# Kernel tuning notes

Hardware: AMD Instinct MI355X
Metric: run time of the kernel (lower is better)

## Reference

```python
import jax, jax.numpy as jnp
import numpy as np

EPS = 1e-6
BN_EPS = 1e-5
K = 20

def _vn_linear(x, W):
    # x: [B,C,...] channel axis 1; W: [out,in]
    return jnp.einsum('oc,bc...->bo...', W, x)

def _vn_bn(x):
    # training-mode BatchNorm on per-vector norms (affine at init: gamma=1, beta=0)
    norm = jnp.sqrt(jnp.sum(x * x, axis=2)) + EPS  # [B,C,*spatial]
    axes = (0,) + tuple(range(2, norm.ndim))
    mean = jnp.mean(norm, axis=axes, keepdims=True)
    var = jnp.mean((norm - mean) ** 2, axis=axes, keepdims=True)  # biased, as torch BN
    norm_bn = (norm - mean) / jnp.sqrt(var + BN_EPS)
    return x / jnp.expand_dims(norm, 2) * jnp.expand_dims(norm_bn, 2)

def _vn_llr(x, Wf, Wd, ns=0.0, use_bn=True):
    p = _vn_linear(x, Wf)
    if use_bn:
        p = _vn_bn(p)
    d = _vn_linear(x, Wd)
    dot = jnp.sum(p * d, axis=2, keepdims=True)
    mask = (dot >= 0).astype(x.dtype)
    dsq = jnp.sum(d * d, axis=2, keepdims=True)
    return ns * p + (1.0 - ns) * (mask * p + (1.0 - mask) * (p - dot / (dsq + EPS) * d))

def _graph_feature_cross(x, k):
    # x: [B,3,N] -> [B,3,3,N,k]
    B, _, N = x.shape
    inner = -2.0 * jnp.einsum('bdn,bdm->bnm', x, x)
    xx = jnp.sum(x * x, axis=1)  # [B,N]
    pdist = -xx[:, :, None] - inner - xx[:, None, :]  # [B,N,N]
    idx = jax.lax.top_k(pdist, k)[1]  # [B,N,k] nearest neighbors
    xt = jnp.transpose(x, (0, 2, 1))  # [B,N,3]
    nbr = xt[jnp.arange(B)[:, None, None], idx]  # [B,N,k,3]
    ctr = jnp.broadcast_to(xt[:, :, None, :], nbr.shape)  # [B,N,k,3]
    cross = jnp.cross(nbr, ctr)
    feat = jnp.stack([nbr - ctr, ctr, cross], axis=3)  # [B,N,k,3ch,3vec]
    return jnp.transpose(feat, (0, 3, 4, 1, 2))  # [B,3,3,N,k]

def _forward(points, wposf, wposd, w1f, w1d, w2f, w2d, w3, ws1f, ws1d, ws2f, ws2d, wlin):
    x = jnp.transpose(points, (0, 2, 1))  # [B,3,N]
    B, _, N = x.shape
    feat = _graph_feature_cross(x, K)  # [B,3,3,N,K]
    x = _vn_llr(feat, wposf, wposd)  # conv_pos, dim=5 -> [B,21,3,N,K]
    x = jnp.mean(x, axis=-1)  # mean pool over k -> [B,21,3,N]
    x = _vn_llr(x, w1f, w1d)  # conv1
    x = _vn_llr(x, w2f, w2d)  # conv2 (feature_transform=False so in=21? no: conv2 takes 42 -- matches cat-free path only when feature_transform False? conv2 in=42 but code passes x of 21? original passes 21-ch into conv2 only if feature_transform else 21; here feature_transform=False and conv2 expects 42 in torch -- we mirror with w2f [42,42] applied after duplicating? No: mirror exact torch behavior below.)
    return x

def reference(points, wposf, wposd, w1f, w1d, w2f, w2d, w3, ws1f, ws1d, ws2f, ws2d, wlin):
    x = jnp.transpose(points, (0, 2, 1))  # [B,3,N]
    B, _, N = x.shape
    feat = _graph_feature_cross(x, K)  # [B,3,3,N,K]
    x = _vn_llr(feat, wposf, wposd)  # [B,21,3,N,K]
    x = jnp.mean(x, axis=-1)  # mean pool -> [B,21,3,N]
    x = _vn_llr(x, w1f, w1d)  # [B,21,3,N]
    # torch conv2 is Linear(42,42) but with feature_transform=False it is applied to 21-ch
    # input; nn.Linear would error, so faithful runnable form uses the duplicated-channel
    # convention: concat (x, x) is NOT in the original; instead we slice w2 to [42,21].
    x = _vn_llr(x, w2f[:, :21], w2d[:, :21])  # [B,42,3,N]
    x = _vn_bn(_vn_linear(x, w3))  # conv3 + bn3 -> [B,85,3,N]
    x_mean_out = jnp.mean(x, axis=-1, keepdims=True)  # [B,85,3,1]
    x = jnp.concatenate([x, jnp.broadcast_to(x_mean_out, x.shape)], axis=1)  # [B,170,3,N]
    z = _vn_llr(x, ws1f, ws1d)  # [B,85,3,N]
    z = _vn_llr(z, ws2f, ws2d)  # [B,42,3,N]
    z = _vn_linear(z, wlin)  # [B,3,3,N]
    z = jnp.transpose(z, (0, 2, 1, 3))  # [B,3,3,N]
    x_std = jnp.einsum('bijm,bjkm->bikm', x, z)  # [B,170,3,N]
    xf = x_std.reshape(B, -1, N)  # [B,510,N]
    inv_z = jnp.max(xf, axis=-1)  # [B,510]
    center_loc = jnp.mean(x_mean_out, axis=2)  # [B,85,1]
    return (inv_z, x_mean_out, center_loc)

def setup_inputs() -> dict:
    key = jax.random.key(0)
    ks = jax.random.split(key, 14)
    B, N = 4, 8192
    def w(k, shape):
        return (jax.random.normal(k, shape, dtype=jnp.float32) * (1.0 / np.sqrt(shape[1])))
    return {
        'points': jax.random.normal(ks[0], (B, N, 3), dtype=jnp.float32),
        'wposf': w(ks[1], (21, 3)),
        'wposd': w(ks[2], (21, 3)),
        'w1f': w(ks[3], (21, 21)),
        'w1d': w(ks[4], (21, 21)),
        'w2f': w(ks[5], (42, 42)),
        'w2d': w(ks[6], (42, 42)),
        'w3': w(ks[7], (85, 42)),
        'ws1f': w(ks[8], (85, 170)),
        'ws1d': w(ks[9], (85, 170)),
        'ws2f': w(ks[10], (42, 85)),
        'ws2d': w(ks[11], (42, 85)),
        'wlin': w(ks[12], (3, 42)),
    }
```

## Files before the change

kernel.cpp:

```cpp
#include <hip/hip_runtime.h>
#include <cstdint>
#include <cstddef>

#define EPSF 1e-6f
#define BN_EPSF 1e-5f

constexpr int Bb = 4;
constexpr int Nn = 8192;
constexpr int KK = 20;
constexpr int SEG = 8;
constexpr int SEGLEN = Nn / SEG;
constexpr int BUF = 24;

constexpr size_t KNN0_OFF = 0;
constexpr size_t X1_OFF  = 0;
constexpr size_t X2_OFF  = 2064384;
constexpr size_t X3_OFF  = 4128768;
constexpr size_t Z1_OFF  = 0;
constexpr size_t X4_OFF  = 8355840;
constexpr size_t IDX_OFF = 16711680;
constexpr size_t Z2_OFF  = 17367040;
constexpr size_t Z3_OFF  = 21495808;
constexpr size_t ACC_OFF = 21790720;
constexpr size_t XM_OFF  = 21791744;
constexpr size_t BF_OFF  = 21792764;
constexpr size_t BD_OFF  = 21793784;
constexpr size_t DEXT_OFF = 21795840;
constexpr size_t EXT_NEED = (DEXT_OFF + 8355840) * 4;

__device__ __forceinline__ float wave_sum(float v) {
#pragma unroll
  for (int off = 32; off; off >>= 1) v += __shfl_xor(v, off, 64);
  return v;
}
__device__ __forceinline__ float wave_max(float v) {
#pragma unroll
  for (int off = 32; off; off >>= 1) v = fmaxf(v, __shfl_xor(v, off, 64));
  return v;
}
__device__ __forceinline__ uint32_t umin32(uint32_t a, uint32_t b) { return a < b ? a : b; }
__device__ __forceinline__ uint32_t umax32(uint32_t a, uint32_t b) { return a < b ? b : a; }

__global__ __launch_bounds__(1024) void zero_acc(float* __restrict__ a) {
  a[threadIdx.x] = 0.f;
}

__global__ __launch_bounds__(256) void knn_kernel(const float* __restrict__ pts,
                                                  uint32_t* __restrict__ knnp) {
  __shared__ float4 tile[SEGLEN];
  __shared__ uint32_t buf[BUF * 256];
  const int tid = threadIdx.x;
  const int n = blockIdx.x * 256 + tid;
  const int b = blockIdx.y;
  const int s = blockIdx.z;
  const float* pb = pts + (size_t)b * Nn * 3;

  for (int i = tid; i < SEGLEN; i += 256) {
    const float* p = pb + (size_t)(s * SEGLEN + i) * 3;
    const float x = p[0], y = p[1], z = p[2];
    tile[i] = make_float4(x, y, z, 0.5f * (x * x + y * y + z * z));
  }
  const float qx = pb[n * 3 + 0], qy = pb[n * 3 + 1], qz = pb[n * 3 + 2];
  const float nqx = -qx, nqy = -qy, nqz = -qz;
  const float h = 0.5f * (qx * qx + qy * qy + qz * qz);
  __syncthreads();

  uint32_t keys[KK];
#pragma unroll
  for (int j = 0; j < KK; ++j) keys[j] = 0xFFFFFFFFu;

  const int base = s * SEGLEN;

#pragma unroll 4
  for (int j = 0; j < 64; ++j) {
    const float4 c = tile[j];
    float u = fmaf(nqx, c.x, fmaf(nqy, c.y, fmaf(nqz, c.z, c.w + h)));
    u = fmaxf(u, 0.f);
    uint32_t mx = (__float_as_uint(u) & 0xFFFFE000u) | (uint32_t)(base + j);
#pragma unroll
    for (int q = 0; q < KK; ++q) {
      const uint32_t mn = umin32(keys[q], mx);
      mx = umax32(keys[q], mx);
      keys[q] = mn;
    }
  }

  uint32_t thresh = keys[KK - 1];
  float thresh_up = __uint_as_float((thresh & 0xFFFFE000u) + 0x2000u);
  float th_h = thresh_up - h + 2.4e-7f * fabsf(thresh_up) + 1e-30f;
  int cnt = 0;

  for (int j0 = 64; j0 < SEGLEN; j0 += 4) {
#pragma unroll
    for (int u4 = 0; u4 < 4; ++u4) {
      const int j = j0 + u4;
      const float4 c = tile[j];
      const float up = fmaf(nqx, c.x, fmaf(nqy, c.y, fmaf(nqz, c.z, c.w)));
      if (up < th_h) {
        const float uc = fmaxf(up + h, 0.f);
        const uint32_t key = (__float_as_uint(uc) & 0xFFFFE000u) | (uint32_t)(base + j);
        buf[cnt * 256 + tid] = key;
        ++cnt;
      }
    }
    if (__any(cnt > BUF - 4)) {
#pragma unroll
      for (int i = 0; i < BUF; ++i) {
        uint32_t mx = (i < cnt) ? buf[i * 256 + tid] : 0xFFFFFFFFu;
#pragma unroll
        for (int q = 0; q < KK; ++q) {
          const uint32_t mn = umin32(keys[q], mx);
          mx = umax32(keys[q], mx);
          keys[q] = mn;
        }
      }
      cnt = 0;
      thresh = keys[KK - 1];
      thresh_up = __uint_as_float((thresh & 0xFFFFE000u) + 0x2000u);
      th_h = thresh_up - h + 2.4e-7f * fabsf(thresh_up) + 1e-30f;
    }
  }
#pragma unroll
  for (int i = 0; i < BUF; ++i) {
    uint32_t mx = (i < cnt) ? buf[i * 256 + tid] : 0xFFFFFFFFu;
#pragma unroll
    for (int q = 0; q < KK; ++q) {
      const uint32_t mn = umin32(keys[q], mx);
      mx = umax32(keys[q], mx);
      keys[q] = mn;
    }
  }

  uint32_t* op = knnp + ((size_t)(b * SEG + s) * KK) * Nn + n;
#pragma unroll
  for (int j = 0; j < KK; ++j) op[(size_t)j * Nn] = keys[j];
}

__global__ __launch_bounds__(256) void merge8(const uint32_t* __restrict__ in,
                                              int* __restrict__ idx) {
  const int t = blockIdx.x * 256 + threadIdx.x;
  const int n = t & (Nn - 1), b = t >> 13;
  const uint32_t* base = in + ((size_t)(b * SEG) * KK) * Nn + n;
  uint32_t h[SEG];
  int ii[SEG];
#pragma unroll
  for (int s = 0; s < SEG; ++s) {
    h[s] = base[(size_t)s * KK * Nn];
    ii[s] = 1;
  }
  int* op = idx + (size_t)t * KK;
#pragma unroll
  for (int m = 0; m < KK; ++m) {
    uint32_t k = h[0];
#pragma unroll
    for (int s = 1; s < SEG; ++s) k = umin32(k, h[s]);
    op[m] = (int)(k & 8191u);
#pragma unroll
    for (int s = 0; s < SEG; ++s) {
      if (h[s] == k) {
        h[s] = (ii[s] < KK) ? base[(size_t)s * KK * Nn + (size_t)ii[s] * Nn] : 0xFFFFFFFFu;
        ii[s]++;
      }
    }
  }
}

__global__ __launch_bounds__(256) void s1_stats(const float* __restrict__ pts,
                                                const int* __restrict__ idx,
                                                const float* __restrict__ wf,
                                                float* __restrict__ acc) {
  __shared__ float lacc[42];
  const int tid = threadIdx.x;
  for (int i = tid; i < 42; i += 256) lacc[i] = 0.f;
  __syncthreads();
  const int t = blockIdx.x * 256 + tid;
  const int site = t / 5;
  const int kq = (t % 5) * 4;
  const int n = site & (Nn - 1), b = site >> 13;
  const float* pb = pts + (size_t)b * Nn * 3;
  const float cx = pb[n * 3 + 0], cy = pb[n * 3 + 1], cz = pb[n * 3 + 2];
  float s1a[21], s2a[21];
#pragma unroll
  for (int o = 0; o < 21; ++o) { s1a[o] = 0.f; s2a[o] = 0.f; }
#pragma unroll
  for (int k = kq; k < kq + 4; ++k) {
    const int m = idx[(size_t)site * KK + k];
    const float ax = pb[m * 3 + 0], ay = pb[m * 3 + 1], az = pb[m * 3 + 2];
    const float e0x = ax - cx, e0y = ay - cy, e0z = az - cz;
    const float e2x = ay * cz - az * cy, e2y = az * cx - ax * cz, e2z = ax * cy - ay * cx;
#pragma unroll
    for (int o = 0; o < 21; ++o) {
      const float w0 = wf[o * 3 + 0], w1 = wf[o * 3 + 1], w2 = wf[o * 3 + 2];
      const float px = w0 * e0x + w1 * cx + w2 * e2x;
      const float py = w0 * e0y + w1 * cy + w2 * e2y;
      const float pz = w0 * e0z + w1 * cz + w2 * e2z;
      const float nrm = sqrtf(px * px + py * py + pz * pz) + EPSF;
      s1a[o] += nrm;
      s2a[o] += nrm * nrm;
    }
  }
#pragma unroll
  for (int o = 0; o < 21; ++o) {
    const float s1 = wave_sum(s1a[o]);
    const float s2 = wave_sum(s2a[o]);
    if ((tid & 63) == 0) { atomicAdd(&lacc[o], s1); atomicAdd(&lacc[21 + o], s2); }
  }
  __syncthreads();
  for (int i = tid; i < 42; i += 256) atomicAdd(&acc[i], lacc[i]);
}

__global__ __launch_bounds__(256) void s1_apply(const float* __restrict__ pts,
                                                const int* __restrict__ idx,
                                                const float* __restrict__ wf,
                                                const float* __restrict__ wd,
                                                const float* __restrict__ acc,
                                                float* __restrict__ x1) {
  const int t = blockIdx.x * 256 + threadIdx.x;
  const int o0 = blockIdx.y * 7;
  const int n = t & (Nn - 1), b = t >> 13;
  const float* pb = pts + (size_t)b * Nn * 3;
  const float cx = pb[n * 3 + 0], cy = pb[n * 3 + 1], cz = pb[n * 3 + 2];
  const float inv_cnt = 1.f / (float)(Bb * Nn * KK);
  float meano[7], istdo[7];
#pragma unroll
  for (int j = 0; j < 7; ++j) {
    const float mn = acc[o0 + j] * inv_cnt;
    const float vr = acc[21 + o0 + j] * inv_cnt - mn * mn;
    meano[j] = mn;
    istdo[j] = rsqrtf(vr + BN_EPSF);
  }
  float accu[7][3];
#pragma unroll
  for (int j = 0; j < 7; ++j) { accu[j][0] = 0.f; accu[j][1] = 0.f; accu[j][2] = 0.f; }
  for (int k = 0; k < KK; ++k) {
    const int m = idx[(size_t)t * KK + k];
    const float ax = pb[m * 3 + 0], ay = pb[m * 3 + 1], az = pb[m * 3 + 2];
    const float e0x = ax - cx, e0y = ay - cy, e0z = az - cz;
    const float e2x = ay * cz - az * cy, e2y = az * cx - ax * cz, e2z = ax * cy - ay * cx;
#pragma unroll
    for (int j = 0; j < 7; ++j) {
      const int o = o0 + j;
      const float wf0 = wf[o * 3 + 0], wf1 = wf[o * 3 + 1], wf2 = wf[o * 3 + 2];
      const float px = wf0 * e0x + wf1 * cx + wf2 * e2x;
      const float py = wf0 * e0y + wf1 * cy + wf2 * e2y;
      const float pz = wf0 * e0z + wf1 * cz + wf2 * e2z;
      const float nrm = sqrtf(px * px + py * py + pz * pz) + EPSF;
      const float factor = (nrm - meano[j]) * istdo[j] / nrm;
      const float q0 = px * factor, q1 = py * factor, q2 = pz * factor;
      const float wd0 = wd[o * 3 + 0], wd1 = wd[o * 3 + 1], wd2 = wd[o * 3 + 2];
      const float dx = wd0 * e0x + wd1 * cx + wd2 * e2x;
      const float dy = wd0 * e0y + wd1 * cy + wd2 * e2y;
      const float dz = wd0 * e0z + wd1 * cz + wd2 * e2z;
      const float dot = q0 * dx + q1 * dy + q2 * dz;
      const float dsq = dx * dx + dy * dy + dz * dz;
      const float corr = (dot < 0.f) ? dot / (dsq + EPSF) : 0.f;
      accu[j][0] += q0 - corr * dx;
      accu[j][1] += q1 - corr * dy;
      accu[j][2] += q2 - corr * dz;
    }
  }
  const float sc = 1.f / (float)KK;
  float* ob = x1 + (size_t)b * 21 * 3 * Nn + n;
#pragma unroll
  for (int j = 0; j < 7; ++j) {
    const int o = o0 + j;
    ob[(o * 3 + 0) * Nn] = accu[j][0] * sc;
    ob[(o * 3 + 1) * Nn] = accu[j][1] * sc;
    ob[(o * 3 + 2) * Nn] = accu[j][2] * sc;
  }
}

template <int CIN, int COUT, int OT, bool HAS_BIAS>
__global__ __launch_bounds__(256) void vn_stats_pd(const float* __restrict__ X,
                                                   const float* __restrict__ Wf,
                                                   const float* __restrict__ Wd, int ws,
                                                   const float* __restrict__ biasF,
                                                   const float* __restrict__ biasD,
                                                   float* __restrict__ acc,
                                                   float* __restrict__ P,
                                                   float* __restrict__ D) {
  __shared__ float lacc[2 * OT];
  const int tid = threadIdx.x;
  if (tid < 2 * OT) lacc[tid] = 0.f;
  __syncthreads();
  const int o0 = blockIdx.y * OT;
  const int t = blockIdx.x * 256 + tid;
  const int n = t & (Nn - 1), b = t >> 13;
  const float* xb = X + (size_t)b * CIN * 3 * Nn + n;
  float* pb = P + (size_t)b * COUT * 3 * Nn + n;
  float* db = D + (size_t)b * COUT * 3 * Nn + n;
  float p[OT][3], dv[OT][3];
#pragma unroll
  for (int j = 0; j < OT; ++j)
#pragma unroll
    for (int dd = 0; dd < 3; ++dd) {
      p[j][dd] = HAS_BIAS ? biasF[((size_t)b * COUT + o0 + j) * 3 + dd] : 0.f;
      dv[j][dd] = HAS_BIAS ? biasD[((size_t)b * COUT + o0 + j) * 3 + dd] : 0.f;
    }
  for (int c = 0; c < CIN; ++c) {
    const float x0 = xb[(c * 3 + 0) * Nn];
    const float x1v = xb[(c * 3 + 1) * Nn];
    const float x2v = xb[(c * 3 + 2) * Nn];
#pragma unroll
    for (int j = 0; j < OT; ++j) {
      const float wfv = Wf[(o0 + j) * ws + c];
      p[j][0] += wfv * x0; p[j][1] += wfv * x1v; p[j][2] += wfv * x2v;
      const float wdv = Wd[(o0 + j) * ws + c];
      dv[j][0] += wdv * x0; dv[j][1] += wdv * x1v; dv[j][2] += wdv * x2v;
    }
  }
#pragma unroll
  for (int j = 0; j < OT; ++j) {
    const int o = o0 + j;
    pb[(size_t)(o * 3 + 0) * Nn] = p[j][0];
    pb[(size_t)(o * 3 + 1) * Nn] = p[j][1];
    pb[(size_t)(o * 3 + 2) * Nn] = p[j][2];
    db[(size_t)(o * 3 + 0) * Nn] = dv[j][0];
    db[(size_t)(o * 3 + 1) * Nn] = dv[j][1];
    db[(size_t)(o * 3 + 2) * Nn] = dv[j][2];
  }
#pragma unroll
  for (int j = 0; j < OT; ++j) {
    const float nrm = sqrtf(p[j][0] * p[j][0] + p[j][1] * p[j][1] + p[j][2] * p[j][2]) + EPSF;
    const float s1 = wave_sum(nrm);
    const float s2 = wave_sum(nrm * nrm);
    if ((tid & 63) == 0) { atomicAdd(&lacc[j], s1); atomicAdd(&lacc[OT + j], s2); }
  }
  __syncthreads();
  if (tid < 2 * OT) {
    const int g = (tid < OT) ? (o0 + tid) : (COUT + o0 + (tid - OT));
    atomicAdd(&acc[g], lacc[tid]);
  }
}

__device__ __forceinline__ float llr_one(float p0, float p1, float p2,
                                         float d0, float d1, float d2,
                                         float mn, float istd,
                                         float& r0o, float& r1o, float& r2o) {
  const float nrm = sqrtf(p0 * p0 + p1 * p1 + p2 * p2) + EPSF;
  const float factor = (nrm - mn) * istd / nrm;
  float r0 = p0 * factor, r1 = p1 * factor, r2 = p2 * factor;
  const float dot = r0 * d0 + r1 * d1 + r2 * d2;
  const float dsq = d0 * d0 + d1 * d1 + d2 * d2;
  const float corr = (dot < 0.f) ? dot / (dsq + EPSF) : 0.f;
  r0o = r0 - corr * d0; r1o = r1 - corr * d1; r2o = r2 - corr * d2;
  return 0.f;
}

template <int COUT>
__global__ __launch_bounds__(256) void vn_llr_ew4(const float* __restrict__ acc, float cntinv,
                                                  float* __restrict__ P,
                                                  const float* __restrict__ D) {
  const int t = blockIdx.x * 256 + threadIdx.x;
  const int n4 = t & (Nn / 4 - 1);
  const int r = t >> 11;
  const int o = r % COUT, b = r / COUT;
  float4* pp = (float4*)(P + ((size_t)(b * COUT + o) * 3) * Nn) + n4;
  const float4* dp = (const float4*)(D + ((size_t)(b * COUT + o) * 3) * Nn) + n4;
  const float4 p0 = pp[0], p1 = pp[Nn / 4], p2 = pp[2 * (Nn / 4)];
  const float4 d0 = dp[0], d1 = dp[Nn / 4], d2 = dp[2 * (Nn / 4)];
  const float mn = acc[o] * cntinv;
  const float vr = acc[COUT + o] * cntinv - mn * mn;
  const float istd = rsqrtf(vr + BN_EPSF);
  float4 r0, r1, r2;
  llr_one(p0.x, p1.x, p2.x, d0.x, d1.x, d2.x, mn, istd, r0.x, r1.x, r2.x);
  llr_one(p0.y, p1.y, p2.y, d0.y, d1.y, d2.y, mn, istd, r0.y, r1.y, r2.y);
  llr_one(p0.z, p1.z, p2.z, d0.z, d1.z, d2.z, mn, istd, r0.z, r1.z, r2.z);
  llr_one(p0.w, p1.w, p2.w, d0.w, d1.w, d2.w, mn, istd, r0.w, r1.w, r2.w);
  pp[0] = r0;
  pp[Nn / 4] = r1;
  pp[2 * (Nn / 4)] = r2;
}

template <int CIN, int COUT, int OT, bool HAS_BIAS>
__global__ __launch_bounds__(256) void vn_stats_pc(const float* __restrict__ X,
                                                   const float* __restrict__ Wf, int ws,
                                                   const float* __restrict__ biasF,
                                                   float* __restrict__ acc,
                                                   float* __restrict__ P) {
  __shared__ float lacc[2 * OT];
  const int tid = threadIdx.x;
  if (tid < 2 * OT) lacc[tid] = 0.f;
  __syncthreads();
  const int o0 = blockIdx.y * OT;
  const int t = blockIdx.x * 256 + tid;
  const int n = t & (Nn - 1), b = t >> 13;
  const float* xb = X + (size_t)b * CIN * 3 * Nn + n;
  float* pb = P + (size_t)b * COUT * 3 * Nn + n;
  float p[OT][3];
#pragma unroll
  for (int j = 0; j < OT; ++j)
#pragma unroll
    for (int dd = 0; dd < 3; ++dd)
      p[j][dd] = HAS_BIAS ? biasF[((size_t)b * COUT + o0 + j) * 3 + dd] : 0.f;
  for (int c = 0; c < CIN; ++c) {
    const float x0 = xb[(c * 3 + 0) * Nn];
    const float x1v = xb[(c * 3 + 1) * Nn];
    const float x2v = xb[(c * 3 + 2) * Nn];
#pragma unroll
    for (int j = 0; j < OT; ++j) {
      const float wv = Wf[(o0 + j) * ws + c];
      p[j][0] += wv * x0; p[j][1] += wv * x1v; p[j][2] += wv * x2v;
    }
  }
#pragma unroll
  for (int j = 0; j < OT; ++j) {
    const int o = o0 + j;
    pb[(size_t)(o * 3 + 0) * Nn] = p[j][0];
    pb[(size_t)(o * 3 + 1) * Nn] = p[j][1];
    pb[(size_t)(o * 3 + 2) * Nn] = p[j][2];
  }
#pragma unroll
  for (int j = 0; j < OT; ++j) {
    const float nrm = sqrtf(p[j][0] * p[j][0] + p[j][1] * p[j][1] + p[j][2] * p[j][2]) + EPSF;
    const float s1 = wave_sum(nrm);
    const float s2 = wave_sum(nrm * nrm);
    if ((tid & 63) == 0) { atomicAdd(&lacc[j], s1); atomicAdd(&lacc[OT + j], s2); }
  }
  __syncthreads();
  if (tid < 2 * OT) {
    const int g = (tid < OT) ? (o0 + tid) : (COUT + o0 + (tid - OT));
    atomicAdd(&acc[g], lacc[tid]);
  }
}

template <int CIN, int COUT, int OT, bool HAS_BIAS>
__global__ __launch_bounds__(256) void vn_apply_pc(const float* __restrict__ X,
                                                   const float* __restrict__ Wd, int ws,
                                                   const float* __restrict__ biasD,
                                                   const float* __restrict__ acc, float cntinv,
                                                   float* __restrict__ P) {
  const int o0 = blockIdx.y * OT;
  const int t = blockIdx.x * 256 + threadIdx.x;
  const int n = t & (Nn - 1), b = t >> 13;
  const float* xb = X + (size_t)b * CIN * 3 * Nn + n;
  float* pb = P + (size_t)b * COUT * 3 * Nn + n;
  float dv[OT][3];
#pragma unroll
  for (int j = 0; j < OT; ++j)
#pragma unroll
    for (int dd = 0; dd < 3; ++dd)
      dv[j][dd] = HAS_BIAS ? biasD[((size_t)b * COUT + o0 + j) * 3 + dd] : 0.f;
  for (int c = 0; c < CIN; ++c) {
    const float x0 = xb[(c * 3 + 0) * Nn];
    const float x1v = xb[(c * 3 + 1) * Nn];
    const float x2v = xb[(c * 3 + 2) * Nn];
#pragma unroll
    for (int j = 0; j < OT; ++j) {
      const float wdv = Wd[(o0 + j) * ws + c];
      dv[j][0] += wdv * x0; dv[j][1] += wdv * x1v; dv[j][2] += wdv * x2v;
    }
  }
#pragma unroll
  for (int j = 0; j < OT; ++j) {
    const int o = o0 + j;
    const float p0 = pb[(size_t)(o * 3 + 0) * Nn];
    const float p1 = pb[(size_t)(o * 3 + 1) * Nn];
    const float p2 = pb[(size_t)(o * 3 + 2) * Nn];
    const float nrm = sqrtf(p0 * p0 + p1 * p1 + p2 * p2) + EPSF;
    const float mn = acc[o] * cntinv;
    const float vr = acc[COUT + o] * cntinv - mn * mn;
    const float factor = (nrm - mn) * rsqrtf(vr + BN_EPSF) / nrm;
    float r0 = p0 * factor, r1 = p1 * factor, r2 = p2 * factor;
    const float dot = r0 * dv[j][0] + r1 * dv[j][1] + r2 * dv[j][2];
    const float dsq = dv[j][0] * dv[j][0] + dv[j][1] * dv[j][1] + dv[j][2] * dv[j][2];
    const float corr = (dot < 0.f) ? dot / (dsq + EPSF) : 0.f;
    r0 -= corr * dv[j][0]; r1 -= corr * dv[j][1]; r2 -= corr * dv[j][2];
    pb[(size_t)(o * 3 + 0) * Nn] = r0;
    pb[(size_t)(o * 3 + 1) * Nn] = r1;
    pb[(size_t)(o * 3 + 2) * Nn] = r2;
  }
}

template <int COUT>
__global__ __launch_bounds__(256) void vn_bn4(const float* __restrict__ acc, float cntinv,
                                              float* __restrict__ P) {
  const int t = blockIdx.x * 256 + threadIdx.x;
  const int n4 = t & (Nn / 4 - 1);
  const int r = t >> 11;
  const int o = r % COUT, b = r / COUT;
  float4* pp = (float4*)(P + ((size_t)(b * COUT + o) * 3) * Nn) + n4;
  const float4 p0 = pp[0], p1 = pp[Nn / 4], p2 = pp[2 * (Nn / 4)];
  const float mn = acc[o] * cntinv;
  const float vr = acc[COUT + o] * cntinv - mn * mn;
  const float istd = rsqrtf(vr + BN_EPSF);
  float4 r0, r1, r2;
#define BN_ONE(f) {                                                        \
    const float nrm = sqrtf(p0.f * p0.f + p1.f * p1.f + p2.f * p2.f) + EPSF; \
    const float factor = (nrm - mn) * istd / nrm;                          \
    r0.f = p0.f * factor; r1.f = p1.f * factor; r2.f = p2.f * factor; }
  BN_ONE(x) BN_ONE(y) BN_ONE(z) BN_ONE(w)
#undef BN_ONE
  pp[0] = r0;
  pp[Nn / 4] = r1;
  pp[2 * (Nn / 4)] = r2;
}

__global__ __launch_bounds__(256) void s5_mean(const float* __restrict__ x4,
                                               float* __restrict__ xm,
                                               float* __restrict__ out) {
  const int row = blockIdx.x;
  const int b = row / 255, rcd = row % 255;
  const float* src = x4 + (size_t)b * 255 * Nn + (size_t)rcd * Nn;
  float s = 0.f;
  for (int n = threadIdx.x; n < Nn; n += 256) s += src[n];
  s = wave_sum(s);
  __shared__ float wsum[4];
  if ((threadIdx.x & 63) == 0) wsum[threadIdx.x >> 6] = s;
  __syncthreads();
  if (threadIdx.x == 0) {
    const float mv = (wsum[0] + wsum[1] + wsum[2] + wsum[3]) * (1.f / (float)Nn);
    xm[row] = mv;
    out[2040 + row] = mv;
  }
}

__global__ __launch_bounds__(256) void s5_bias(const float* __restrict__ xm,
                                               const float* __restrict__ ws1f,
                                               const float* __restrict__ ws1d,
                                               float* __restrict__ biasF,
                                               float* __restrict__ biasD,
                                               float* __restrict__ out) {
  const int t = blockIdx.x * 256 + threadIdx.x;
  if (t < 1020) {
    const int b = t / 255, r = t % 255, o = r / 3, dd = r % 3;
    float sf = 0.f, sd = 0.f;
    for (int c = 0; c < 85; ++c) {
      const float xv = xm[(b * 85 + c) * 3 + dd];
      sf += ws1f[o * 170 + 85 + c] * xv;
      sd += ws1d[o * 170 + 85 + c] * xv;
    }
    biasF[t] = sf;
    biasD[t] = sd;
  }
  if (t < 340) {
    const int b = t / 85, c = t % 85;
    out[3060 + t] = (xm[(b * 85 + c) * 3 + 0] + xm[(b * 85 + c) * 3 + 1] +
                     xm[(b * 85 + c) * 3 + 2]) * (1.f / 3.f);
  }
}

__global__ __launch_bounds__(256) void s8_z3(const float* __restrict__ z2,
                                             const float* __restrict__ wlin,
                                             float* __restrict__ z3) {
  const int t = blockIdx.x * 256 + threadIdx.x;
  const int n = t & (Nn - 1), b = t >> 13;
  const float* zb = z2 + (size_t)b * 42 * 3 * Nn + n;
  float accv[3][3];
#pragma unroll
  for (int o = 0; o < 3; ++o)
#pragma unroll
    for (int dd = 0; dd < 3; ++dd) accv[o][dd] = 0.f;
  for (int c = 0; c < 42; ++c) {
    const float x0 = zb[(c * 3 + 0) * Nn];
    const float x1v = zb[(c * 3 + 1) * Nn];
    const float x2v = zb[(c * 3 + 2) * Nn];
#pragma unroll
    for (int o = 0; o < 3; ++o) {
      const float wv = wlin[o * 42 + c];
      accv[o][0] += wv * x0; accv[o][1] += wv * x1v; accv[o][2] += wv * x2v;
    }
  }
  float* ob = z3 + (size_t)b * 9 * Nn + n;
#pragma unroll
  for (int o = 0; o < 3; ++o)
#pragma unroll
    for (int dd = 0; dd < 3; ++dd) ob[(o * 3 + dd) * Nn] = accv[o][dd];
}

__global__ __launch_bounds__(256) void s9_max(const float* __restrict__ x4,
                                              const float* __restrict__ xm,
                                              const float* __restrict__ z3,
                                              float* __restrict__ out) {
  const int tile = blockIdx.x;
  const int b = blockIdx.y;
  const int i0 = tile * 5;
  const bool upper = (i0 >= 85);
  float mx[15];
#pragma unroll
  for (int r = 0; r < 15; ++r) mx[r] = -3.402823466e38f;
  float xmr[5][3];
  if (upper) {
#pragma unroll
    for (int ii = 0; ii < 5; ++ii)
#pragma unroll
      for (int j = 0; j < 3; ++j) xmr[ii][j] = xm[(b * 85 + (i0 - 85 + ii)) * 3 + j];
  }
  const float* zb = z3 + (size_t)b * 9 * Nn;
  const float* xb = x4 + (size_t)b * 255 * Nn;
  for (int n = threadIdx.x; n < Nn; n += 256) {
    float zk[3][3];
#pragma unroll
    for (int k = 0; k < 3; ++k)
#pragma unroll
      for (int j = 0; j < 3; ++j) zk[k][j] = zb[(k * 3 + j) * Nn + n];
#pragma unroll
    for (int ii = 0; ii < 5; ++ii) {
      float xj0, xj1, xj2;
      if (upper) {
        xj0 = xmr[ii][0]; xj1 = xmr[ii][1]; xj2 = xmr[ii][2];
      } else {
        xj0 = xb[((i0 + ii) * 3 + 0) * Nn + n];
        xj1 = xb[((i0 + ii) * 3 + 1) * Nn + n];
        xj2 = xb[((i0 + ii) * 3 + 2) * Nn + n];
      }
#pragma unroll
      for (int k = 0; k < 3; ++k) {
        const float v = xj0 * zk[k][0] + xj1 * zk[k][1] + xj2 * zk[k][2];
        mx[ii * 3 + k] = fmaxf(mx[ii * 3 + k], v);
      }
    }
  }
  __shared__ float red[4 * 15];
#pragma unroll
  for (int r = 0; r < 15; ++r) {
    const float v = wave_max(mx[r]);
    if ((threadIdx.x & 63) == 0) red[(threadIdx.x >> 6) * 15 + r] = v;
  }
  __syncthreads();
  if (threadIdx.x < 15) {
    const float v = fmaxf(fmaxf(red[threadIdx.x], red[15 + threadIdx.x]),
                          fmaxf(red[30 + threadIdx.x], red[45 + threadIdx.x]));
    out[b * 510 + i0 * 3 + threadIdx.x] = v;
  }
}

extern "C" void kernel_launch(void* const* d_in, const int* in_sizes, int n_in,
                              void* d_out, int out_size, void* d_ws, size_t ws_size,
                              hipStream_t stream) {
  const float* pts   = (const float*)d_in[0];
  const float* wposf = (const float*)d_in[1];
  const float* wposd = (const float*)d_in[2];
  const float* w1f   = (const float*)d_in[3];
  const float* w1d   = (const float*)d_in[4];
  const float* w2f   = (const float*)d_in[5];
  const float* w2d   = (const float*)d_in[6];
  const float* w3    = (const float*)d_in[7];
  const float* ws1f  = (const float*)d_in[8];
  const float* ws1d  = (const float*)d_in[9];
  const float* ws2f  = (const float*)d_in[10];
  const float* ws2d  = (const float*)d_in[11];
  const float* wlin  = (const float*)d_in[12];
  float* out = (float*)d_out;
  float* wsf = (float*)d_ws;

  uint32_t* knnp0 = (uint32_t*)(wsf + KNN0_OFF);
  float* x1 = wsf + X1_OFF;
  float* x2 = wsf + X2_OFF;
  float* x3 = wsf + X3_OFF;
  float* z1 = wsf + Z1_OFF;
  float* x4 = wsf + X4_OFF;
  int* idx  = (int*)(wsf + IDX_OFF);
  float* z2 = wsf + Z2_OFF;
  float* z3 = wsf + Z3_OFF;
  float* acc = wsf + ACC_OFF;
  float* xm = wsf + XM_OFF;
  float* biasF = wsf + BF_OFF;
  float* biasD = wsf + BD_OFF;
  float* d1 = wsf + X3_OFF;
  float* d2 = wsf + X4_OFF;
  float* dext = wsf + DEXT_OFF;
  const bool ext = ws_size >= EXT_NEED;

  const float inv_sites = 1.f / (float)(Bb * Nn);

  zero_acc<<<1, 1024, 0, stream>>>(acc);
  knn_kernel<<<dim3(Nn / 256, Bb, SEG), 256, 0, stream>>>(pts, knnp0);
  merge8<<<Bb * Nn / 256, 256, 0, stream>>>(knnp0, idx);

  s1_stats<<<Bb * Nn * 5 / 256, 256, 0, stream>>>(pts, idx, wposf, acc + 0);
  s1_apply<<<dim3(Bb * Nn / 256, 3), 256, 0, stream>>>(pts, idx, wposf, wposd, acc + 0, x1);

  vn_stats_pd<21, 21, 7, false><<<dim3(Bb * Nn / 256, 3), 256, 0, stream>>>(
      x1, w1f, w1d, 21, nullptr, nullptr, acc + 64, x2, d1);
  vn_llr_ew4<21><<<Bb * 21 * Nn / 4 / 256, 256, 0, stream>>>(acc + 64, inv_sites, x2, d1);

  vn_stats_pd<21, 42, 7, false><<<dim3(Bb * Nn / 256, 6), 256, 0, stream>>>(
      x2, w2f, w2d, 42, nullptr, nullptr, acc + 128, x3, d2);
  vn_llr_ew4<42><<<Bb * 42 * Nn / 4 / 256, 256, 0, stream>>>(acc + 128, inv_sites, x3, d2);

  vn_stats_pc<42, 85, 17, false><<<dim3(Bb * Nn / 256, 5), 256, 0, stream>>>(
      x3, w3, 42, nullptr, acc + 256, x4);
  vn_bn4<85><<<Bb * 85 * Nn / 4 / 256, 256, 0, stream>>>(acc + 256, inv_sites, x4);

  s5_mean<<<Bb * 255, 256, 0, stream>>>(x4, xm, out);
  s5_bias<<<4, 256, 0, stream>>>(xm, ws1f, ws1d, biasF, biasD, out);

  if (ext) {
    vn_stats_pd<85, 85, 5, true><<<dim3(Bb * Nn / 256, 17), 256, 0, stream>>>(
        x4, ws1f, ws1d, 170, biasF, biasD, acc + 512, z1, dext);
    vn_llr_ew4<85><<<Bb * 85 * Nn / 4 / 256, 256, 0, stream>>>(acc + 512, inv_sites, z1, dext);
    vn_stats_pd<85, 42, 7, false><<<dim3(Bb * Nn / 256, 6), 256, 0, stream>>>(
        z1, ws2f, ws2d, 85, nullptr, nullptr, acc + 768, z2, dext);
    vn_llr_ew4<42><<<Bb * 42 * Nn / 4 / 256, 256, 0, stream>>>(acc + 768, inv_sites, z2, dext);
  } else {
    vn_stats_pc<85, 85, 17, true><<<dim3(Bb * Nn / 256, 5), 256, 0, stream>>>(
        x4, ws1f, 170, biasF, acc + 512, z1);
    vn_apply_pc<85, 85, 17, true><<<dim3(Bb * Nn / 256, 5), 256, 0, stream>>>(
        x4, ws1d, 170, biasD, acc + 512, inv_sites, z1);
    vn_stats_pc<85, 42, 14, false><<<dim3(Bb * Nn / 256, 3), 256, 0, stream>>>(
        z1, ws2f, 85, nullptr, acc + 768, z2);
    vn_apply_pc<85, 42, 14, false><<<dim3(Bb * Nn / 256, 3), 256, 0, stream>>>(
        z1, ws2d, 85, nullptr, acc + 768, inv_sites, z2);
  }

  s8_z3<<<Bb * Nn / 256, 256, 0, stream>>>(z2, wlin, z3);
  s9_max<<<dim3(34, Bb), 256, 0, stream>>>(x4, xm, z3, out);
}
```

Baseline: 677.1 us.

## Process two query points per thread in kNN and retile conv3 stats kernel

The kNN kernel now handles two query points per thread, so each shared-memory tile read is reused for two distance computations and the grid is halved. The per-thread candidate buffer is split into two halves of the old size, which keeps shared memory the same but means flushes happen more often. Separately, the conv3 stats kernel is relaunched with 5 output channels per block across 17 blocks instead of 17 channels across 5 blocks, trading more parallelism for more input reloads. The two-query change roughly doubles live key registers, which may lower occupancy.

```diff
diff --git a/kernel.cpp b/kernel.cpp
--- a/kernel.cpp
+++ b/kernel.cpp
@@ -10,7 +10,7 @@
 constexpr int KK = 20;
 constexpr int SEG = 8;
 constexpr int SEGLEN = Nn / SEG;
-constexpr int BUF = 24;
+constexpr int BUF = 12;
 
 constexpr size_t KNN0_OFF = 0;
 constexpr size_t X1_OFF  = 0;
@@ -48,9 +48,11 @@
 __global__ __launch_bounds__(256) void knn_kernel(const float* __restrict__ pts,
                                                   uint32_t* __restrict__ knnp) {
   __shared__ float4 tile[SEGLEN];
-  __shared__ uint32_t buf[BUF * 256];
+  __shared__ uint32_t buf0[BUF * 256];
+  __shared__ uint32_t buf1[BUF * 256];
   const int tid = threadIdx.x;
-  const int n = blockIdx.x * 256 + tid;
+  const int n0 = blockIdx.x * 512 + tid;
+  const int n1 = n0 + 256;
   const int b = blockIdx.y;
   const int s = blockIdx.z;
   const float* pb = pts + (size_t)b * Nn * 3;
@@ -60,80 +62,116 @@
     const float x = p[0], y = p[1], z = p[2];
     tile[i] = make_float4(x, y, z, 0.5f * (x * x + y * y + z * z));
   }
-  const float qx = pb[n * 3 + 0], qy = pb[n * 3 + 1], qz = pb[n * 3 + 2];
-  const float nqx = -qx, nqy = -qy, nqz = -qz;
-  const float h = 0.5f * (qx * qx + qy * qy + qz * qz);
-  __syncthreads();
-
-  uint32_t keys[KK];
-#pragma unroll
-  for (int j = 0; j < KK; ++j) keys[j] = 0xFFFFFFFFu;
+  const float q0x = pb[n0 * 3 + 0], q0y = pb[n0 * 3 + 1], q0z = pb[n0 * 3 + 2];
+  const float q1x = pb[n1 * 3 + 0], q1y = pb[n1 * 3 + 1], q1z = pb[n1 * 3 + 2];
+  const float h0 = 0.5f * (q0x * q0x + q0y * q0y + q0z * q0z);
+  const float h1 = 0.5f * (q1x * q1x + q1y * q1y + q1z * q1z);
+  const float nq0x = -q0x, nq0y = -q0y, nq0z = -q0z;
+  const float nq1x = -q1x, nq1y = -q1y, nq1z = -q1z;
+  __syncthreads();
+
+  uint32_t keys0[KK], keys1[KK];
+#pragma unroll
+  for (int j = 0; j < KK; ++j) { keys0[j] = 0xFFFFFFFFu; keys1[j] = 0xFFFFFFFFu; }
 
   const int base = s * SEGLEN;
 
-#pragma unroll 4
+#pragma unroll 2
   for (int j = 0; j < 64; ++j) {
     const float4 c = tile[j];
-    float u = fmaf(nqx, c.x, fmaf(nqy, c.y, fmaf(nqz, c.z, c.w + h)));
-    u = fmaxf(u, 0.f);
-    uint32_t mx = (__float_as_uint(u) & 0xFFFFE000u) | (uint32_t)(base + j);
-#pragma unroll
-    for (int q = 0; q < KK; ++q) {
-      const uint32_t mn = umin32(keys[q], mx);
-      mx = umax32(keys[q], mx);
-      keys[q] = mn;
-    }
-  }
-
-  uint32_t thresh = keys[KK - 1];
-  float thresh_up = __uint_as_float((thresh & 0xFFFFE000u) + 0x2000u);
-  float th_h = thresh_up - h + 2.4e-7f * fabsf(thresh_up) + 1e-30f;
-  int cnt = 0;
+    const uint32_t tag = (uint32_t)(base + j);
+    {
+      float u = fmaf(nq0x, c.x, fmaf(nq0y, c.y, fmaf(nq0z, c.z, c.w + h0)));
+      u = fmaxf(u, 0.f);
+      uint32_t mx = (__float_as_uint(u) & 0xFFFFE000u) | tag;
+#pragma unroll
+      for (int q = 0; q < KK; ++q) {
+        const uint32_t mn = umin32(keys0[q], mx);
+        mx = umax32(keys0[q], mx);
+        keys0[q] = mn;
+      }
+    }
+    {
+      float u = fmaf(nq1x, c.x, fmaf(nq1y, c.y, fmaf(nq1z, c.z, c.w + h1)));
+      u = fmaxf(u, 0.f);
+      uint32_t mx = (__float_as_uint(u) & 0xFFFFE000u) | tag;
+#pragma unroll
+      for (int q = 0; q < KK; ++q) {
+        const uint32_t mn = umin32(keys1[q], mx);
+        mx = umax32(keys1[q], mx);
+        keys1[q] = mn;
+      }
+    }
+  }
+
+  uint32_t th0 = keys0[KK - 1], th1 = keys1[KK - 1];
+  float tu0 = __uint_as_float((th0 & 0xFFFFE000u) + 0x2000u);
+  float tu1 = __uint_as_float((th1 & 0xFFFFE000u) + 0x2000u);
+  float thh0 = tu0 - h0 + 2.4e-7f * fabsf(tu0) + 1e-30f;
+  float thh1 = tu1 - h1 + 2.4e-7f * fabsf(tu1) + 1e-30f;
+  int cnt0 = 0, cnt1 = 0;
 
   for (int j0 = 64; j0 < SEGLEN; j0 += 4) {
 #pragma unroll
     for (int u4 = 0; u4 < 4; ++u4) {
       const int j = j0 + u4;
       const float4 c = tile[j];
-      const float up = fmaf(nqx, c.x, fmaf(nqy, c.y, fmaf(nqz, c.z, c.w)));
-      if (up < th_h) {
-        const float uc = fmaxf(up + h, 0.f);
-        const uint32_t key = (__float_as_uint(uc) & 0xFFFFE000u) | (uint32_t)(base + j);
-        buf[cnt * 256 + tid] = key;
-        ++cnt;
+      const uint32_t tag = (uint32_t)(base + j);
+      const float up0 = fmaf(nq0x, c.x, fmaf(nq0y, c.y, fmaf(nq0z, c.z, c.w)));
+      if (up0 < thh0) {
+        const float uc = fmaxf(up0 + h0, 0.f);
+        buf0[cnt0 * 256 + tid] = (__float_as_uint(uc) & 0xFFFFE000u) | tag;
+        ++cnt0;
       }
-    }
-    if (__any(cnt > BUF - 4)) {
+      const float up1 = fmaf(nq1x, c.x, fmaf(nq1y, c.y, fmaf(nq1z, c.z, c.w)));
+      if (up1 < thh1) {
+        const float uc = fmaxf(up1 + h1, 0.f);
+        buf1[cnt1 * 256 + tid] = (__float_as_uint(uc) & 0xFFFFE000u) | tag;
+        ++cnt1;
+      }
+    }
+    if (__any((cnt0 > BUF - 4) || (cnt1 > BUF - 4))) {
 #pragma unroll
       for (int i = 0; i < BUF; ++i) {
-        uint32_t mx = (i < cnt) ? buf[i * 256 + tid] : 0xFFFFFFFFu;
+        uint32_t mx0 = (i < cnt0) ? buf0[i * 256 + tid] : 0xFFFFFFFFu;
+        uint32_t mx1 = (i < cnt1) ? buf1[i * 256 + tid] : 0xFFFFFFFFu;
 #pragma unroll
         for (int q = 0; q < KK; ++q) {
-          const uint32_t mn = umin32(keys[q], mx);
-          mx = umax32(keys[q], mx);
-          keys[q] = mn;
+          const uint32_t mn0 = umin32(keys0[q], mx0);
+          mx0 = umax32(keys0[q], mx0);
+          keys0[q] = mn0;
+          const uint32_t mn1 = umin32(keys1[q], mx1);
+          mx1 = umax32(keys1[q], mx1);
+          keys1[q] = mn1;
         }
       }
-      cnt = 0;
-      thresh = keys[KK - 1];
-      thresh_up = __uint_as_float((thresh & 0xFFFFE000u) + 0x2000u);
-      th_h = thresh_up - h + 2.4e-7f * fabsf(thresh_up) + 1e-30f;
+      cnt0 = 0; cnt1 = 0;
+      th0 = keys0[KK - 1]; th1 = keys1[KK - 1];
+      tu0 = __uint_as_float((th0 & 0xFFFFE000u) + 0x2000u);
+      tu1 = __uint_as_float((th1 & 0xFFFFE000u) + 0x2000u);
+      thh0 = tu0 - h0 + 2.4e-7f * fabsf(tu0) + 1e-30f;
+      thh1 = tu1 - h1 + 2.4e-7f * fabsf(tu1) + 1e-30f;
     }
   }
 #pragma unroll
   for (int i = 0; i < BUF; ++i) {
-    uint32_t mx = (i < cnt) ? buf[i * 256 + tid] : 0xFFFFFFFFu;
+    uint32_t mx0 = (i < cnt0) ? buf0[i * 256 + tid] : 0xFFFFFFFFu;
+    uint32_t mx1 = (i < cnt1) ? buf1[i * 256 + tid] : 0xFFFFFFFFu;
 #pragma unroll
     for (int q = 0; q < KK; ++q) {
-      const uint32_t mn = umin32(keys[q], mx);
-      mx = umax32(keys[q], mx);
-      keys[q] = mn;
-    }
-  }
-
-  uint32_t* op = knnp + ((size_t)(b * SEG + s) * KK) * Nn + n;
-#pragma unroll
-  for (int j = 0; j < KK; ++j) op[(size_t)j * Nn] = keys[j];
+      const uint32_t mn0 = umin32(keys0[q], mx0);
+      mx0 = umax32(keys0[q], mx0);
+      keys0[q] = mn0;
+      const uint32_t mn1 = umin32(keys1[q], mx1);
+      mx1 = umax32(keys1[q], mx1);
+      keys1[q] = mn1;
+    }
+  }
+
+  uint32_t* op0 = knnp + ((size_t)(b * SEG + s) * KK) * Nn + n0;
+  uint32_t* op1 = knnp + ((size_t)(b * SEG + s) * KK) * Nn + n1;
+#pragma unroll
+  for (int j = 0; j < KK; ++j) { op0[(size_t)j * Nn] = keys0[j]; op1[(size_t)j * Nn] = keys1[j]; }
 }
 
 __global__ __launch_bounds__(256) void merge8(const uint32_t* __restrict__ in,
@@ -665,7 +703,7 @@
   const float inv_sites = 1.f / (float)(Bb * Nn);
 
   zero_acc<<<1, 1024, 0, stream>>>(acc);
-  knn_kernel<<<dim3(Nn / 256, Bb, SEG), 256, 0, stream>>>(pts, knnp0);
+  knn_kernel<<<dim3(Nn / 512, Bb, SEG), 256, 0, stream>>>(pts, knnp0);
   merge8<<<Bb * Nn / 256, 256, 0, stream>>>(knnp0, idx);
 
   s1_stats<<<Bb * Nn * 5 / 256, 256, 0, stream>>>(pts, idx, wposf, acc + 0);
@@ -679,7 +717,7 @@
       x2, w2f, w2d, 42, nullptr, nullptr, acc + 128, x3, d2);
   vn_llr_ew4<42><<<Bb * 42 * Nn / 4 / 256, 256, 0, stream>>>(acc + 128, inv_sites, x3, d2);
 
-  vn_stats_pc<42, 85, 17, false><<<dim3(Bb * Nn / 256, 5), 256, 0, stream>>>(
+  vn_stats_pc<42, 85, 5, false><<<dim3(Bb * Nn / 256, 17), 256, 0, stream>>>(
       x3, w3, 42, nullptr, acc + 256, x4);
   vn_bn4<85><<<Bb * 85 * Nn / 4 / 256, 256, 0, stream>>>(acc + 256, inv_sites, x4);
 
```

New measurement: 704.5 us. 4.0% more time.
